# Kernel optimization log

Measured on AMD Instinct MI355X. Metric: run time of the kernel, lower is better.

The kernel has to match this reference:

```python
import jax, jax.numpy as jnp
import numpy as np

TAU = 1.0            # module's self.temperature (set externally in the repo)
NUM_EMBED = 1024     # num_embeddings
EPS = 1e-10


def setup_inputs() -> dict:
    key = jax.random.key(0)
    k1, k2, k3 = jax.random.split(key, 3)
    B, S, N, D = 8, 2048, 1024, 512
    logits = jax.random.normal(k1, (B, S, N), dtype=jnp.float32)
    # uniform samples for deterministic gumbel noise g = -log(-log(u))
    u = jax.random.uniform(k2, (B, S, N), dtype=jnp.float32,
                           minval=1e-6, maxval=1.0 - 1e-6)
    embed = jax.random.normal(k3, (N, D), dtype=jnp.float32) * 0.02
    return {"logits": logits, "u": u, "embed": embed}


def reference(logits, u, embed):
    # F.gumbel_softmax(logits, tau, dim=2, hard=True)
    gumbel = -jnp.log(-jnp.log(u))                      # [B,S,N]
    y_soft = jax.nn.softmax((logits + gumbel) / TAU, axis=2)
    ind = jnp.argmax(y_soft, axis=2)                    # [B,S] int
    y_hard = jax.nn.one_hot(ind, logits.shape[2], dtype=y_soft.dtype)
    # straight-through: hard value, soft gradient
    one_hot = y_hard + y_soft - jax.lax.stop_gradient(y_soft)
    # einsum('b s n, n d -> b s d') with the codebook
    z_q = jnp.einsum('bsn,nd->bsd', one_hot, embed)     # [B,S,D]
    qy = jax.nn.softmax(logits, axis=2)
    diff = -jnp.log(qy * NUM_EMBED + EPS) / qy          # [B,S,N]
    return z_q, diff, ind
```

## Files before the change

kernel.cpp:

```cpp
#include <hip/hip_runtime.h>
#include <math.h>

#define N_EMB 1024
#define D_EMB 512
#define EPS_Q 1e-10f

__global__ __launch_bounds__(256) void gumbel_quantize_kernel(
    const float* __restrict__ logits,
    const float* __restrict__ u,
    const float* __restrict__ embed,
    float*       __restrict__ zq,
    float*       __restrict__ diff,
    float*       __restrict__ indf)
{
    const int row  = blockIdx.x;
    const int t    = threadIdx.x;
    const int lane = t & 63;
    const int wave = t >> 6;
    const size_t rbase = (size_t)row * N_EMB;

    const float4 l4 = ((const float4*)(logits + rbase))[t];
    const float4 u4 = ((const float4*)(u      + rbase))[t];

    float lv[4] = {l4.x, l4.y, l4.z, l4.w};
    float uv[4] = {u4.x, u4.y, u4.z, u4.w};

    float smax = -INFINITY; int sidx = 0;
    float lmax = -INFINITY;
    #pragma unroll
    for (int j = 0; j < 4; ++j) {
        const float g  = -logf(-logf(uv[j]));
        const float sc = lv[j] + g;
        const int   idx = t * 4 + j;
        if (sc > smax) { smax = sc; sidx = idx; }
        lmax = fmaxf(lmax, lv[j]);
    }

    #pragma unroll
    for (int off = 32; off > 0; off >>= 1) {
        const float v2 = __shfl_xor(smax, off, 64);
        const int   i2 = __shfl_xor(sidx, off, 64);
        if (v2 > smax || (v2 == smax && i2 < sidx)) { smax = v2; sidx = i2; }
        lmax = fmaxf(lmax, __shfl_xor(lmax, off, 64));
    }

    __shared__ float s_v[4];
    __shared__ int   s_i[4];
    __shared__ float s_m[4];
    __shared__ int   s_bi;
    __shared__ float s_lm;
    __shared__ float s_sum[4];

    if (lane == 0) { s_v[wave] = smax; s_i[wave] = sidx; s_m[wave] = lmax; }
    __syncthreads();
    if (t == 0) {
        float bv = s_v[0]; int bi = s_i[0]; float bm = s_m[0];
        #pragma unroll
        for (int w = 1; w < 4; ++w) {
            if (s_v[w] > bv || (s_v[w] == bv && s_i[w] < bi)) { bv = s_v[w]; bi = s_i[w]; }
            bm = fmaxf(bm, s_m[w]);
        }
        s_bi = bi; s_lm = bm;
    }
    __syncthreads();
    const int   ind = s_bi;
    const float m   = s_lm;

    float e[4];
    float psum = 0.f;
    #pragma unroll
    for (int j = 0; j < 4; ++j) { e[j] = expf(lv[j] - m); psum += e[j]; }
    #pragma unroll
    for (int off = 32; off > 0; off >>= 1) psum += __shfl_xor(psum, off, 64);
    if (lane == 0) s_sum[wave] = psum;
    __syncthreads();
    const float sum = s_sum[0] + s_sum[1] + s_sum[2] + s_sum[3];
    const float inv = 1.0f / sum;

    float d[4];
    #pragma unroll
    for (int j = 0; j < 4; ++j) {
        const float qy = e[j] * inv;
        d[j] = -logf(qy * (float)N_EMB + EPS_Q) / qy;
    }
    ((float4*)(diff + rbase))[t] = make_float4(d[0], d[1], d[2], d[3]);

    const float2* erow = (const float2*)(embed + (size_t)ind * D_EMB);
    float2*       zrow = (float2*)(zq + (size_t)row * D_EMB);
    zrow[t] = erow[t];

    if (t == 0) indf[row] = (float)ind;
}

extern "C" void kernel_launch(void* const* d_in, const int* in_sizes, int n_in,
                              void* d_out, int out_size, void* d_ws, size_t ws_size,
                              hipStream_t stream) {
    const float* logits = (const float*)d_in[0];
    const float* u      = (const float*)d_in[1];
    const float* embed  = (const float*)d_in[2];

    const int rows = in_sizes[0] / N_EMB;

    float* out  = (float*)d_out;
    float* zq   = out;
    float* diff = zq + (size_t)rows * D_EMB;
    float* indf = diff + (size_t)rows * N_EMB;

    gumbel_quantize_kernel<<<rows, 256, 0, stream>>>(logits, u, embed, zq, diff, indf);
}
```

Baseline: 201.4 us.

## Map one row per wavefront and simplify diff math

Each 64-lane wavefront now handles a whole row of 1024 elements, with four rows per block. This drops all shared-memory reductions and block barriers in favour of wave shuffles. The diff computation replaces the per-element log and divide with one log per row plus a fast reciprocal, rewriting -log(qy*N)/qy algebraically. The fast exp and reciprocal intrinsics are used, and the epsilon term is dropped, which may change accuracy slightly for tiny qy. It also assumes the row count is divisible by four.

```diff
diff --git a/kernel.cpp b/kernel.cpp
--- a/kernel.cpp
+++ b/kernel.cpp
@@ -3,7 +3,6 @@
 
 #define N_EMB 1024
 #define D_EMB 512
-#define EPS_Q 1e-10f
 
 __global__ __launch_bounds__(256) void gumbel_quantize_kernel(
     const float* __restrict__ logits,
@@ -13,27 +12,40 @@
     float*       __restrict__ diff,
     float*       __restrict__ indf)
 {
-    const int row  = blockIdx.x;
-    const int t    = threadIdx.x;
-    const int lane = t & 63;
-    const int wave = t >> 6;
+    const int lane = threadIdx.x & 63;
+    const int wave = threadIdx.x >> 6;
+    const int row  = blockIdx.x * 4 + wave;
     const size_t rbase = (size_t)row * N_EMB;
 
-    const float4 l4 = ((const float4*)(logits + rbase))[t];
-    const float4 u4 = ((const float4*)(u      + rbase))[t];
+    const float4* lp = (const float4*)(logits + rbase);
+    const float4* up = (const float4*)(u      + rbase);
 
-    float lv[4] = {l4.x, l4.y, l4.z, l4.w};
-    float uv[4] = {u4.x, u4.y, u4.z, u4.w};
+    float4 l4[4], u4[4];
+    #pragma unroll
+    for (int c = 0; c < 4; ++c) l4[c] = lp[c * 64 + lane];
+    #pragma unroll
+    for (int c = 0; c < 4; ++c) u4[c] = up[c * 64 + lane];
+
+    float lv[16];
+    #pragma unroll
+    for (int c = 0; c < 4; ++c) {
+        lv[c*4+0] = l4[c].x; lv[c*4+1] = l4[c].y;
+        lv[c*4+2] = l4[c].z; lv[c*4+3] = l4[c].w;
+    }
 
     float smax = -INFINITY; int sidx = 0;
     float lmax = -INFINITY;
     #pragma unroll
-    for (int j = 0; j < 4; ++j) {
-        const float g  = -logf(-logf(uv[j]));
-        const float sc = lv[j] + g;
-        const int   idx = t * 4 + j;
-        if (sc > smax) { smax = sc; sidx = idx; }
-        lmax = fmaxf(lmax, lv[j]);
+    for (int c = 0; c < 4; ++c) {
+        const float us[4] = {u4[c].x, u4[c].y, u4[c].z, u4[c].w};
+        #pragma unroll
+        for (int j = 0; j < 4; ++j) {
+            const float g  = -logf(-logf(us[j]));
+            const float sc = lv[c*4+j] + g;
+            const int idx  = c * 256 + lane * 4 + j;
+            if (sc > smax) { smax = sc; sidx = idx; }
+            lmax = fmaxf(lmax, lv[c*4+j]);
+        }
     }
 
     #pragma unroll
@@ -43,53 +55,37 @@
         if (v2 > smax || (v2 == smax && i2 < sidx)) { smax = v2; sidx = i2; }
         lmax = fmaxf(lmax, __shfl_xor(lmax, off, 64));
     }
+    const int   ind = sidx;
+    const float m   = lmax;
 
-    __shared__ float s_v[4];
-    __shared__ int   s_i[4];
-    __shared__ float s_m[4];
-    __shared__ int   s_bi;
-    __shared__ float s_lm;
-    __shared__ float s_sum[4];
-
-    if (lane == 0) { s_v[wave] = smax; s_i[wave] = sidx; s_m[wave] = lmax; }
-    __syncthreads();
-    if (t == 0) {
-        float bv = s_v[0]; int bi = s_i[0]; float bm = s_m[0];
-        #pragma unroll
-        for (int w = 1; w < 4; ++w) {
-            if (s_v[w] > bv || (s_v[w] == bv && s_i[w] < bi)) { bv = s_v[w]; bi = s_i[w]; }
-            bm = fmaxf(bm, s_m[w]);
-        }
-        s_bi = bi; s_lm = bm;
-    }
-    __syncthreads();
-    const int   ind = s_bi;
-    const float m   = s_lm;
-
-    float e[4];
+    float e[16];
     float psum = 0.f;
     #pragma unroll
-    for (int j = 0; j < 4; ++j) { e[j] = expf(lv[j] - m); psum += e[j]; }
+    for (int j = 0; j < 16; ++j) { e[j] = __expf(lv[j] - m); psum += e[j]; }
     #pragma unroll
     for (int off = 32; off > 0; off >>= 1) psum += __shfl_xor(psum, off, 64);
-    if (lane == 0) s_sum[wave] = psum;
-    __syncthreads();
-    const float sum = s_sum[0] + s_sum[1] + s_sum[2] + s_sum[3];
+    const float sum = psum;
     const float inv = 1.0f / sum;
+    const float L = logf((float)N_EMB * inv);
 
-    float d[4];
+    float4* dp = (float4*)(diff + rbase);
     #pragma unroll
-    for (int j = 0; j < 4; ++j) {
-        const float qy = e[j] * inv;
-        d[j] = -logf(qy * (float)N_EMB + EPS_Q) / qy;
+    for (int c = 0; c < 4; ++c) {
+        float d[4];
+        #pragma unroll
+        for (int j = 0; j < 4; ++j) {
+            const int k = c * 4 + j;
+            d[j] = -((lv[k] - m) + L) * sum * __builtin_amdgcn_rcpf(e[k]);
+        }
+        dp[c * 64 + lane] = make_float4(d[0], d[1], d[2], d[3]);
     }
-    ((float4*)(diff + rbase))[t] = make_float4(d[0], d[1], d[2], d[3]);
 
-    const float2* erow = (const float2*)(embed + (size_t)ind * D_EMB);
-    float2*       zrow = (float2*)(zq + (size_t)row * D_EMB);
-    zrow[t] = erow[t];
+    const float4* erow = (const float4*)(embed + (size_t)ind * D_EMB);
+    float4*       zrow = (float4*)(zq + (size_t)row * D_EMB);
+    #pragma unroll
+    for (int c = 0; c < 2; ++c) zrow[c * 64 + lane] = erow[c * 64 + lane];
 
-    if (t == 0) indf[row] = (float)ind;
+    if (lane == 0) indf[row] = (float)ind;
 }
 
 extern "C" void kernel_launch(void* const* d_in, const int* in_sizes, int n_in,
@@ -106,5 +102,6 @@
     float* diff = zq + (size_t)rows * D_EMB;
     float* indf = diff + (size_t)rows * N_EMB;
 
-    gumbel_quantize_kernel<<<rows, 256, 0, stream>>>(logits, u, embed, zq, diff, indf);
+    gumbel_quantize_kernel<<<rows / 4, 256, 0, stream>>>(logits, u, embed,
+                                                         zq, diff, indf);
 }
```

Result: slower. 206.4 us (+2.5%).
